# Kernel optimization log

Measured on AMD Instinct MI355X. Metric: run time of the kernel, lower is better.

## Reference

```python
import jax, jax.numpy as jnp
import numpy as np

B, LQ, LK, D, H = 8, 1024, 1024, 1024, 8
DH = D // H  # per-head dim (att_units // num_heads, and V head dim since V = k)
LN_EPS = 1e-5


def setup_inputs() -> dict:
    key = jax.random.key(0)
    ks = jax.random.split(key, 8)
    s = 1.0 / np.sqrt(D)
    return {
        "q": jax.random.normal(ks[0], (B, LQ, D), dtype=jnp.float32),
        "k": jax.random.normal(ks[1], (B, LK, D), dtype=jnp.float32),
        "Wq": jax.random.normal(ks[2], (D, D), dtype=jnp.float32) * s,
        "bq": jnp.zeros((D,), dtype=jnp.float32),
        "Wk": jax.random.normal(ks[3], (D, D), dtype=jnp.float32) * s,
        "bk": jnp.zeros((D,), dtype=jnp.float32),
        "ln_gamma": jnp.ones((D,), dtype=jnp.float32),
        "ln_beta": jnp.zeros((D,), dtype=jnp.float32),
    }


def _layer_norm(x, gamma, beta):
    mu = jnp.mean(x, axis=-1, keepdims=True)
    var = jnp.mean(jnp.square(x - mu), axis=-1, keepdims=True)
    return (x - mu) * jax.lax.rsqrt(var + LN_EPS) * gamma + beta


def reference(q, k, Wq, bq, Wk, bk, ln_gamma, ln_beta):
    # q: [B, LQ, D], k: [B, LK, D]
    Q = q @ Wq + bq                      # [B, LQ, D]
    K = k @ Wk + bk                      # [B, LK, D]
    V = k                                # V is the raw key input (no projection)
    Qh = Q.reshape(B, LQ, H, DH)         # split(att_units//H, -1)+concat(0) == head reshape
    Kh = K.reshape(B, LK, H, DH)
    Vh = V.reshape(B, LK, H, DH)
    sim = jnp.einsum("bqhd,bkhd->bhqk", Qh, Kh) / np.sqrt(DH).astype(np.float32)
    attn = jax.nn.softmax(sim, axis=-1)  # [B, H, LQ, LK]
    att_h = jnp.einsum("bhqk,bkhd->bqhd", attn, Vh).reshape(B, LQ, D)
    att_h = att_h * 0.1 + q * 0.9        # residual blend
    att_h = _layer_norm(att_h, ln_gamma, ln_beta)
    return att_h  # ff_units_list == [] -> ff is None -> ff_h = att_h
```

## Files before the change

kernel.cpp:

```cpp
#include <hip/hip_runtime.h>
#include <hip/hip_bf16.h>
#include <cstdint>

#define BATCH 8
#define SEQ   1024
#define DMODEL 1024
#define NHEAD 8
#define DHEAD 128

using short8 = __attribute__((ext_vector_type(8))) short;
using f32x4  = __attribute__((ext_vector_type(4))) float;
typedef unsigned short u16;

__device__ inline u16 f2bf(float f) {
    union { float f; uint32_t u; } v; v.f = f;
    uint32_t r = (v.u + 0x7FFFu + ((v.u >> 16) & 1u)) >> 16;
    return (u16)r;
}

__device__ inline float exp2_fast(float x) { return __builtin_amdgcn_exp2f(x); }

__device__ inline uint32_t cvtpk_bf16(float a, float b) {
    uint32_t r;
    asm("v_cvt_pk_bf16_f32 %0, %1, %2" : "=v"(r) : "v"(a), "v"(b));
    return r;
}

#define GLL16(g, l)                                                                        \
    __builtin_amdgcn_global_load_lds((__attribute__((address_space(1))) const uint32_t*)(g), \
                                     (__attribute__((address_space(3))) uint32_t*)(l), 16, 0, 0)

__global__ __launch_bounds__(256) void conv_bf16(const float* __restrict__ q,
                                                 u16* __restrict__ dst) {
    size_t e = ((size_t)blockIdx.x * 256 + threadIdx.x) * 8;
    float4 a = *(const float4*)(q + e);
    float4 b = *(const float4*)(q + e + 4);
    uint4 r;
    r.x = cvtpk_bf16(a.x, a.y);
    r.y = cvtpk_bf16(a.z, a.w);
    r.z = cvtpk_bf16(b.x, b.y);
    r.w = cvtpk_bf16(b.z, b.w);
    *(uint4*)(dst + e) = r;
}

__global__ void transpose_conv(const float* __restrict__ Wq,
                               const float* __restrict__ Wk,
                               const float* __restrict__ kin,
                               u16* __restrict__ WqT,
                               u16* __restrict__ WkT,
                               u16* __restrict__ Vt,
                               u16* __restrict__ kb) {
    __shared__ float tile[32][33];
    int z = blockIdx.z;
    const float* src;
    u16* dst;
    u16* sdst = nullptr;
    if (z == 0)      { src = Wq; dst = WqT; }
    else if (z == 1) { src = Wk; dst = WkT; }
    else {
        src  = kin + (size_t)(z - 2) * DMODEL * SEQ;
        dst  = Vt  + (size_t)(z - 2) * DMODEL * SEQ;
        sdst = kb  + (size_t)(z - 2) * DMODEL * SEQ;
    }
    int x  = blockIdx.x * 32 + threadIdx.x;
    int y0 = blockIdx.y * 32;
    for (int i = threadIdx.y; i < 32; i += 8) {
        float v = src[(size_t)(y0 + i) * 1024 + x];
        tile[i][threadIdx.x] = v;
        if (sdst) sdst[(size_t)(y0 + i) * 1024 + x] = f2bf(v);
    }
    __syncthreads();
    int xo  = y0 + threadIdx.x;
    int yo0 = blockIdx.x * 32;
    for (int i = threadIdx.y; i < 32; i += 8)
        dst[(size_t)(yo0 + i) * 1024 + xo] = f2bf(tile[threadIdx.x][i]);
}

__global__ __launch_bounds__(256, 4) void gemm_dual(const u16* __restrict__ Aq,
                                                    const u16* __restrict__ Ak,
                                                    const u16* __restrict__ BTq,
                                                    const u16* __restrict__ BTk,
                                                    const float* __restrict__ biasq,
                                                    const float* __restrict__ biask,
                                                    u16* __restrict__ Outq,
                                                    u16* __restrict__ Outk) {
    __shared__ __align__(16) u16 As[2][128 * 32];
    __shared__ __align__(16) u16 Bs[2][128 * 32];

    int bid = blockIdx.x;
    int half = bid >> 9;
    int b2 = bid & 511;
    const u16* A  = half ? Ak  : Aq;
    const u16* BT = half ? BTk : BTq;
    const float* bias = half ? biask : biasq;
    u16* Out = half ? Outk : Outq;
    float scale = half ? 1.0f : (0.08838834764831845f * 1.4426950408889634f);

    int swz = (b2 & 7) * 64 + (b2 >> 3);
    int mt = swz >> 3, nt = swz & 7;
    int m0 = mt * 128, n0 = nt * 128;

    int t = threadIdx.x, lane = t & 63, w = t >> 6;
    int wm = w >> 1, wn = w & 1;
    int lr = lane & 15, lg = lane >> 4;

    const u16* pa[2];
    const u16* pb[2];
#pragma unroll
    for (int i = 0; i < 2; ++i) {
        int L = (w * 2 + i) * 64 + lane;
        int rp = L >> 3, ss = L & 7;
        int u = ss ^ (rp & 7);
        int row = (rp << 1) | (u >> 2);
        int g = u & 3;
        pa[i] = A  + (size_t)(m0 + row) * 1024 + g * 8;
        pb[i] = BT + (size_t)(n0 + row) * 1024 + g * 8;
    }
    int aoff[4], boff[4];
#pragma unroll
    for (int f = 0; f < 4; ++f) {
        int rowA = wm * 64 + f * 16 + lr;
        int sA = (((rowA & 1) << 2) | lg) ^ ((rowA >> 1) & 7);
        aoff[f] = (rowA >> 1) * 64 + sA * 8;
        int rowB = wn * 64 + f * 16 + lr;
        int sB = (((rowB & 1) << 2) | lg) ^ ((rowB >> 1) & 7);
        boff[f] = (rowB >> 1) * 64 + sB * 8;
    }

    f32x4 acc[4][4] = {};

#define GSTAGE(buf)                                         \
    {                                                       \
        _Pragma("unroll")                                   \
        for (int i = 0; i < 2; ++i) {                       \
            GLL16(pa[i], &As[buf][(w * 2 + i) * 512]);      \
            GLL16(pb[i], &Bs[buf][(w * 2 + i) * 512]);      \
            pa[i] += 32;                                    \
            pb[i] += 32;                                    \
        }                                                   \
    }

    GSTAGE(0);
    __syncthreads();

    int cur = 0;
    for (int k0 = 0; k0 < DMODEL; k0 += 32) {
        if (k0 + 32 < DMODEL) GSTAGE(cur ^ 1);
        short8 af[4], bfr[4];
#pragma unroll
        for (int f = 0; f < 4; ++f) {
            af[f]  = *(const short8*)&As[cur][aoff[f]];
            bfr[f] = *(const short8*)&Bs[cur][boff[f]];
        }
        __builtin_amdgcn_s_setprio(1);
#pragma unroll
        for (int fm = 0; fm < 4; ++fm)
#pragma unroll
            for (int fn = 0; fn < 4; ++fn)
                acc[fm][fn] = __builtin_amdgcn_mfma_f32_16x16x32_bf16(af[fm], bfr[fn], acc[fm][fn], 0, 0, 0);
        __builtin_amdgcn_s_setprio(0);
        __syncthreads();
        cur ^= 1;
    }
#undef GSTAGE

#pragma unroll
    for (int fn = 0; fn < 4; ++fn) {
        int col = n0 + wn * 64 + fn * 16 + lr;
        float bv = bias[col];
#pragma unroll
        for (int fm = 0; fm < 4; ++fm)
#pragma unroll
            for (int j = 0; j < 4; ++j) {
                int row = m0 + wm * 64 + fm * 16 + lg * 4 + j;
                Out[(size_t)row * 1024 + col] = f2bf((acc[fm][fn][j] + bv) * scale);
            }
    }
}

__global__ __launch_bounds__(512, 4) void attn_kernel(const u16* __restrict__ Qb,
                                                      const u16* __restrict__ Kb,
                                                      const u16* __restrict__ Vt,
                                                      float* __restrict__ AO) {
    __shared__ __align__(16) u16 Kbuf[2][64 * 128];
    __shared__ __align__(16) u16 Vbuf[2][128 * 64];
    __shared__ __align__(16) u16 Pl[8][16 * 64];

    int bid = blockIdx.x;
    int swz = (bid & 7) * 64 + (bid >> 3);
    int bh  = swz >> 3;
    int qt  = swz & 7;
    int b = bh >> 3, h = bh & 7;
    int q0 = qt * 128;

    int t = threadIdx.x, lane = t & 63, w = t >> 6;
    int lr = lane & 15, lg = lane >> 4;

    short8 qf[4];
    {
        size_t qbase = (size_t)(b * SEQ + q0 + w * 16 + lr) * 1024 + h * DHEAD;
#pragma unroll
        for (int kk = 0; kk < 4; ++kk)
            qf[kk] = *(const short8*)&Qb[qbase + kk * 32 + lg * 8];
    }

    float m_i = -1e30f, l_loc = 0.f;
    f32x4 o[8] = {};
    u16* Pw = &Pl[w][0];
    const int pwrow = lr * 64;
    const int lx = lr & 7;

#define STAGE(nb, kk0)                                                                   \
    {                                                                                    \
        _Pragma("unroll")                                                                \
        for (int i = 0; i < 2; ++i) {                                                    \
            int g = (w * 2 + i) * 64 + lane;                                             \
            int row = g >> 4, cp = g & 15;                                               \
            int c = cp ^ (row & 7);                                                      \
            const u16* src = Kb + ((size_t)(b * SEQ + (kk0) + row) * 1024 + h * 128 + c * 8); \
            GLL16(src, &Kbuf[nb][(w * 2 + i) * 512]);                                    \
        }                                                                                \
        _Pragma("unroll")                                                                \
        for (int i = 0; i < 2; ++i) {                                                    \
            int g = (w * 2 + i) * 64 + lane;                                             \
            int d = g >> 3, cp = g & 7;                                                  \
            int c = cp ^ (d & 7);                                                        \
            const u16* src = Vt + ((size_t)(bh * 128 + d) * 1024 + (kk0) + c * 8);       \
            GLL16(src, &Vbuf[nb][(w * 2 + i) * 512]);                                    \
        }                                                                                \
    }

    STAGE(0, 0);
    __syncthreads();

    int cur = 0;
    for (int k0 = 0; k0 < SEQ; k0 += 64) {
        if (k0 + 64 < SEQ) STAGE(cur ^ 1, k0 + 64);

        const u16* Kc = &Kbuf[cur][0];
        f32x4 s[4] = {};
        __builtin_amdgcn_s_setprio(1);
#pragma unroll
        for (int fn = 0; fn < 4; ++fn) {
            int krow = (fn * 16 + lr) * 128;
#pragma unroll
            for (int kk = 0; kk < 4; ++kk) {
                short8 kf = *(const short8*)&Kc[krow + (((kk * 4 + lg) ^ lx) << 3)];
                s[fn] = __builtin_amdgcn_mfma_f32_16x16x32_bf16(kf, qf[kk], s[fn], 0, 0, 0);
            }
        }
        __builtin_amdgcn_s_setprio(0);

        float pm0 = fmaxf(fmaxf(s[0][0], s[0][1]), fmaxf(s[0][2], s[0][3]));
        float pm1 = fmaxf(fmaxf(s[1][0], s[1][1]), fmaxf(s[1][2], s[1][3]));
        float pm2 = fmaxf(fmaxf(s[2][0], s[2][1]), fmaxf(s[2][2], s[2][3]));
        float pm3 = fmaxf(fmaxf(s[3][0], s[3][1]), fmaxf(s[3][2], s[3][3]));
        float pmax = fmaxf(fmaxf(pm0, pm1), fmaxf(pm2, pm3));

        if (__any(pmax > m_i + 11.5416f)) {
            float rm = pmax;
            rm = fmaxf(rm, __shfl_xor(rm, 16));
            rm = fmaxf(rm, __shfl_xor(rm, 32));
            float mnew = fmaxf(m_i, rm);
            float alpha = exp2_fast(m_i - mnew);
            m_i = mnew;
            l_loc *= alpha;
#pragma unroll
            for (int db = 0; db < 8; ++db) o[db] *= alpha;
        }

        float p[4][4];
        float ls0 = 0.f, ls1 = 0.f, ls2 = 0.f, ls3 = 0.f;
#pragma unroll
        for (int j = 0; j < 4; ++j) {
            p[0][j] = exp2_fast(s[0][j] - m_i); ls0 += p[0][j];
            p[1][j] = exp2_fast(s[1][j] - m_i); ls1 += p[1][j];
            p[2][j] = exp2_fast(s[2][j] - m_i); ls2 += p[2][j];
            p[3][j] = exp2_fast(s[3][j] - m_i); ls3 += p[3][j];
        }
        l_loc += (ls0 + ls1) + (ls2 + ls3);

#pragma unroll
        for (int fn = 0; fn < 4; ++fn) {
            uint2 pk;
            pk.x = cvtpk_bf16(p[fn][0], p[fn][1]);
            pk.y = cvtpk_bf16(p[fn][2], p[fn][3]);
            int idx = pwrow + (((fn * 2 + (lg >> 1)) ^ lx) << 3) + ((lg & 1) << 2);
            *(uint2*)&Pw[idx] = pk;
        }

        const u16* Vc = &Vbuf[cur][0];
        short8 pf0 = *(const short8*)&Pw[pwrow + ((lg ^ lx) << 3)];
        short8 pf1 = *(const short8*)&Pw[pwrow + (((4 + lg) ^ lx) << 3)];
        __builtin_amdgcn_s_setprio(1);
#pragma unroll
        for (int db = 0; db < 8; ++db) {
            int vr = (db * 16 + lr) * 64;
            short8 v0 = *(const short8*)&Vc[vr + ((lg ^ lx) << 3)];
            short8 v1 = *(const short8*)&Vc[vr + (((4 + lg) ^ lx) << 3)];
            o[db] = __builtin_amdgcn_mfma_f32_16x16x32_bf16(v0, pf0, o[db], 0, 0, 0);
            o[db] = __builtin_amdgcn_mfma_f32_16x16x32_bf16(v1, pf1, o[db], 0, 0, 0);
        }
        __builtin_amdgcn_s_setprio(0);

        __syncthreads();
        cur ^= 1;
    }

    float lt = l_loc;
    lt += __shfl_xor(lt, 16);
    lt += __shfl_xor(lt, 32);
    float inv = 1.f / lt;
    size_t obase = (size_t)(b * SEQ + q0 + w * 16 + lr) * 1024 + h * DHEAD + lg * 4;
#pragma unroll
    for (int db = 0; db < 8; ++db) {
        float4 ov;
        ov.x = o[db][0] * inv;
        ov.y = o[db][1] * inv;
        ov.z = o[db][2] * inv;
        ov.w = o[db][3] * inv;
        *(float4*)&AO[obase + db * 16] = ov;
    }
#undef STAGE
}

__global__ __launch_bounds__(256) void ln_kernel(float* __restrict__ AO,
                                                 const float* __restrict__ qin,
                                                 const float* __restrict__ gamma,
                                                 const float* __restrict__ beta,
                                                 float* __restrict__ out) {
    __shared__ float red[8];
    int row = blockIdx.x;
    int t = threadIdx.x;
    size_t base = (size_t)row * 1024 + t * 4;

    float4 a = *(const float4*)&AO[base];
    float4 qq = *(const float4*)&qin[base];
    float x0 = a.x * 0.1f + qq.x * 0.9f;
    float x1 = a.y * 0.1f + qq.y * 0.9f;
    float x2 = a.z * 0.1f + qq.z * 0.9f;
    float x3 = a.w * 0.1f + qq.w * 0.9f;

    float s  = x0 + x1 + x2 + x3;
    float s2 = x0 * x0 + x1 * x1 + x2 * x2 + x3 * x3;
    for (int d = 1; d < 64; d <<= 1) {
        s  += __shfl_xor(s, d);
        s2 += __shfl_xor(s2, d);
    }
    int w = t >> 6, lane = t & 63;
    if (lane == 0) { red[w] = s; red[4 + w] = s2; }
    __syncthreads();
    s  = red[0] + red[1] + red[2] + red[3];
    s2 = red[4] + red[5] + red[6] + red[7];

    float mu   = s * (1.f / 1024.f);
    float var  = s2 * (1.f / 1024.f) - mu * mu;
    float rstd = rsqrtf(var + 1e-5f);

    float4 g  = *(const float4*)&gamma[t * 4];
    float4 be = *(const float4*)&beta[t * 4];
    float4 o;
    o.x = (x0 - mu) * rstd * g.x + be.x;
    o.y = (x1 - mu) * rstd * g.y + be.y;
    o.z = (x2 - mu) * rstd * g.z + be.z;
    o.w = (x3 - mu) * rstd * g.w + be.w;
    *(float4*)&out[base] = o;
}

extern "C" void kernel_launch(void* const* d_in, const int* in_sizes, int n_in,
                              void* d_out, int out_size, void* d_ws, size_t ws_size,
                              hipStream_t stream) {
    const float* q     = (const float*)d_in[0];
    const float* k     = (const float*)d_in[1];
    const float* Wq    = (const float*)d_in[2];
    const float* bq    = (const float*)d_in[3];
    const float* Wk    = (const float*)d_in[4];
    const float* bk    = (const float*)d_in[5];
    const float* gamma = (const float*)d_in[6];
    const float* beta  = (const float*)d_in[7];
    float* out = (float*)d_out;

    char* ws = (char*)d_ws;
    u16* WqT = (u16*)ws;
    u16* WkT = (u16*)(ws + (size_t)(2  << 20));
    u16* Qb  = (u16*)(ws + (size_t)(4  << 20));
    u16* Kb  = (u16*)(ws + (size_t)(20 << 20));
    u16* Vt  = (u16*)(ws + (size_t)(36 << 20));

    u16* qb = (u16*)d_out;
    u16* kb = qb + (size_t)8 * 1024 * 1024;

    conv_bf16<<<4096, 256, 0, stream>>>(q, qb);

    transpose_conv<<<dim3(32, 32, 2 + BATCH), dim3(32, 8), 0, stream>>>(Wq, Wk, k, WqT, WkT, Vt, kb);

    gemm_dual<<<1024, 256, 0, stream>>>(qb, kb, WqT, WkT, bq, bk, Qb, Kb);

    attn_kernel<<<512, 512, 0, stream>>>(Qb, Kb, Vt, out);

    ln_kernel<<<8192, 256, 0, stream>>>(out, q, gamma, beta, out);
}
```

Baseline: 133.3 us.

## Process two query subtiles per wave to double K/V reuse in attention

Each wave now handles 32 query rows (two 16-row subtiles) instead of 16, so each block covers 256 queries and the grid halves to 256 blocks. Every K and V fragment read from shared memory feeds two MFMAs, which halves LDS traffic and global K/V staging per query. The cost is twice the accumulator registers, so launch bounds drop to 2 blocks per CU, and with only 256 blocks on a 256-CU part there is one block per CU, leaving less latency hiding.

After: 132.7 us. No clear change (-0.5%).

```diff
diff --git a/kernel.cpp b/kernel.cpp
--- a/kernel.cpp
+++ b/kernel.cpp
@@ -178,35 +178,39 @@
     }
 }
 
-__global__ __launch_bounds__(512, 4) void attn_kernel(const u16* __restrict__ Qb,
+__global__ __launch_bounds__(512, 2) void attn_kernel(const u16* __restrict__ Qb,
                                                       const u16* __restrict__ Kb,
                                                       const u16* __restrict__ Vt,
                                                       float* __restrict__ AO) {
     __shared__ __align__(16) u16 Kbuf[2][64 * 128];
     __shared__ __align__(16) u16 Vbuf[2][128 * 64];
-    __shared__ __align__(16) u16 Pl[8][16 * 64];
+    __shared__ __align__(16) u16 Pl[8][2][16 * 64];
 
     int bid = blockIdx.x;
-    int swz = (bid & 7) * 64 + (bid >> 3);
-    int bh  = swz >> 3;
-    int qt  = swz & 7;
+    int swz = (bid & 7) * 32 + (bid >> 3);
+    int bh  = swz >> 2;
+    int qt  = swz & 3;
     int b = bh >> 3, h = bh & 7;
-    int q0 = qt * 128;
+    int q0 = qt * 256;
 
     int t = threadIdx.x, lane = t & 63, w = t >> 6;
     int lr = lane & 15, lg = lane >> 4;
 
-    short8 qf[4];
+    short8 qfA[4], qfB[4];
     {
-        size_t qbase = (size_t)(b * SEQ + q0 + w * 16 + lr) * 1024 + h * DHEAD;
-#pragma unroll
-        for (int kk = 0; kk < 4; ++kk)
-            qf[kk] = *(const short8*)&Qb[qbase + kk * 32 + lg * 8];
-    }
-
-    float m_i = -1e30f, l_loc = 0.f;
-    f32x4 o[8] = {};
-    u16* Pw = &Pl[w][0];
+        size_t qa = (size_t)(b * SEQ + q0 + w * 32 + lr) * 1024 + h * DHEAD;
+        size_t qbB = qa + (size_t)16 * 1024;
+#pragma unroll
+        for (int kk = 0; kk < 4; ++kk) {
+            qfA[kk] = *(const short8*)&Qb[qa  + kk * 32 + lg * 8];
+            qfB[kk] = *(const short8*)&Qb[qbB + kk * 32 + lg * 8];
+        }
+    }
+
+    float mA = -1e30f, lA = 0.f, mB = -1e30f, lB = 0.f;
+    f32x4 oA[8] = {}, oB[8] = {};
+    u16* PwA = &Pl[w][0][0];
+    u16* PwB = &Pl[w][1][0];
     const int pwrow = lr * 64;
     const int lx = lr & 7;
 
@@ -238,7 +242,7 @@
         if (k0 + 64 < SEQ) STAGE(cur ^ 1, k0 + 64);
 
         const u16* Kc = &Kbuf[cur][0];
-        f32x4 s[4] = {};
+        f32x4 sA[4] = {}, sB[4] = {};
         __builtin_amdgcn_s_setprio(1);
 #pragma unroll
         for (int fn = 0; fn < 4; ++fn) {
@@ -246,60 +250,100 @@
 #pragma unroll
             for (int kk = 0; kk < 4; ++kk) {
                 short8 kf = *(const short8*)&Kc[krow + (((kk * 4 + lg) ^ lx) << 3)];
-                s[fn] = __builtin_amdgcn_mfma_f32_16x16x32_bf16(kf, qf[kk], s[fn], 0, 0, 0);
+                sA[fn] = __builtin_amdgcn_mfma_f32_16x16x32_bf16(kf, qfA[kk], sA[fn], 0, 0, 0);
+                sB[fn] = __builtin_amdgcn_mfma_f32_16x16x32_bf16(kf, qfB[kk], sB[fn], 0, 0, 0);
             }
         }
         __builtin_amdgcn_s_setprio(0);
 
-        float pm0 = fmaxf(fmaxf(s[0][0], s[0][1]), fmaxf(s[0][2], s[0][3]));
-        float pm1 = fmaxf(fmaxf(s[1][0], s[1][1]), fmaxf(s[1][2], s[1][3]));
-        float pm2 = fmaxf(fmaxf(s[2][0], s[2][1]), fmaxf(s[2][2], s[2][3]));
-        float pm3 = fmaxf(fmaxf(s[3][0], s[3][1]), fmaxf(s[3][2], s[3][3]));
-        float pmax = fmaxf(fmaxf(pm0, pm1), fmaxf(pm2, pm3));
-
-        if (__any(pmax > m_i + 11.5416f)) {
-            float rm = pmax;
-            rm = fmaxf(rm, __shfl_xor(rm, 16));
-            rm = fmaxf(rm, __shfl_xor(rm, 32));
-            float mnew = fmaxf(m_i, rm);
-            float alpha = exp2_fast(m_i - mnew);
-            m_i = mnew;
-            l_loc *= alpha;
-#pragma unroll
-            for (int db = 0; db < 8; ++db) o[db] *= alpha;
-        }
-
-        float p[4][4];
-        float ls0 = 0.f, ls1 = 0.f, ls2 = 0.f, ls3 = 0.f;
-#pragma unroll
-        for (int j = 0; j < 4; ++j) {
-            p[0][j] = exp2_fast(s[0][j] - m_i); ls0 += p[0][j];
-            p[1][j] = exp2_fast(s[1][j] - m_i); ls1 += p[1][j];
-            p[2][j] = exp2_fast(s[2][j] - m_i); ls2 += p[2][j];
-            p[3][j] = exp2_fast(s[3][j] - m_i); ls3 += p[3][j];
-        }
-        l_loc += (ls0 + ls1) + (ls2 + ls3);
-
-#pragma unroll
-        for (int fn = 0; fn < 4; ++fn) {
-            uint2 pk;
-            pk.x = cvtpk_bf16(p[fn][0], p[fn][1]);
-            pk.y = cvtpk_bf16(p[fn][2], p[fn][3]);
-            int idx = pwrow + (((fn * 2 + (lg >> 1)) ^ lx) << 3) + ((lg & 1) << 2);
-            *(uint2*)&Pw[idx] = pk;
+        {
+            float pm0 = fmaxf(fmaxf(sA[0][0], sA[0][1]), fmaxf(sA[0][2], sA[0][3]));
+            float pm1 = fmaxf(fmaxf(sA[1][0], sA[1][1]), fmaxf(sA[1][2], sA[1][3]));
+            float pm2 = fmaxf(fmaxf(sA[2][0], sA[2][1]), fmaxf(sA[2][2], sA[2][3]));
+            float pm3 = fmaxf(fmaxf(sA[3][0], sA[3][1]), fmaxf(sA[3][2], sA[3][3]));
+            float pmax = fmaxf(fmaxf(pm0, pm1), fmaxf(pm2, pm3));
+            if (__any(pmax > mA + 11.5416f)) {
+                float rm = pmax;
+                rm = fmaxf(rm, __shfl_xor(rm, 16));
+                rm = fmaxf(rm, __shfl_xor(rm, 32));
+                float mnew = fmaxf(mA, rm);
+                float alpha = exp2_fast(mA - mnew);
+                mA = mnew;
+                lA *= alpha;
+#pragma unroll
+                for (int db = 0; db < 8; ++db) oA[db] *= alpha;
+            }
+            float p[4][4];
+            float ls0 = 0.f, ls1 = 0.f, ls2 = 0.f, ls3 = 0.f;
+#pragma unroll
+            for (int j = 0; j < 4; ++j) {
+                p[0][j] = exp2_fast(sA[0][j] - mA); ls0 += p[0][j];
+                p[1][j] = exp2_fast(sA[1][j] - mA); ls1 += p[1][j];
+                p[2][j] = exp2_fast(sA[2][j] - mA); ls2 += p[2][j];
+                p[3][j] = exp2_fast(sA[3][j] - mA); ls3 += p[3][j];
+            }
+            lA += (ls0 + ls1) + (ls2 + ls3);
+#pragma unroll
+            for (int fn = 0; fn < 4; ++fn) {
+                uint2 pk;
+                pk.x = cvtpk_bf16(p[fn][0], p[fn][1]);
+                pk.y = cvtpk_bf16(p[fn][2], p[fn][3]);
+                int idx = pwrow + (((fn * 2 + (lg >> 1)) ^ lx) << 3) + ((lg & 1) << 2);
+                *(uint2*)&PwA[idx] = pk;
+            }
+        }
+        {
+            float pm0 = fmaxf(fmaxf(sB[0][0], sB[0][1]), fmaxf(sB[0][2], sB[0][3]));
+            float pm1 = fmaxf(fmaxf(sB[1][0], sB[1][1]), fmaxf(sB[1][2], sB[1][3]));
+            float pm2 = fmaxf(fmaxf(sB[2][0], sB[2][1]), fmaxf(sB[2][2], sB[2][3]));
+            float pm3 = fmaxf(fmaxf(sB[3][0], sB[3][1]), fmaxf(sB[3][2], sB[3][3]));
+            float pmax = fmaxf(fmaxf(pm0, pm1), fmaxf(pm2, pm3));
+            if (__any(pmax > mB + 11.5416f)) {
+                float rm = pmax;
+                rm = fmaxf(rm, __shfl_xor(rm, 16));
+                rm = fmaxf(rm, __shfl_xor(rm, 32));
+                float mnew = fmaxf(mB, rm);
+                float alpha = exp2_fast(mB - mnew);
+                mB = mnew;
+                lB *= alpha;
+#pragma unroll
+                for (int db = 0; db < 8; ++db) oB[db] *= alpha;
+            }
+            float p[4][4];
+            float ls0 = 0.f, ls1 = 0.f, ls2 = 0.f, ls3 = 0.f;
+#pragma unroll
+            for (int j = 0; j < 4; ++j) {
+                p[0][j] = exp2_fast(sB[0][j] - mB); ls0 += p[0][j];
+                p[1][j] = exp2_fast(sB[1][j] - mB); ls1 += p[1][j];
+                p[2][j] = exp2_fast(sB[2][j] - mB); ls2 += p[2][j];
+                p[3][j] = exp2_fast(sB[3][j] - mB); ls3 += p[3][j];
+            }
+            lB += (ls0 + ls1) + (ls2 + ls3);
+#pragma unroll
+            for (int fn = 0; fn < 4; ++fn) {
+                uint2 pk;
+                pk.x = cvtpk_bf16(p[fn][0], p[fn][1]);
+                pk.y = cvtpk_bf16(p[fn][2], p[fn][3]);
+                int idx = pwrow + (((fn * 2 + (lg >> 1)) ^ lx) << 3) + ((lg & 1) << 2);
+                *(uint2*)&PwB[idx] = pk;
+            }
         }
 
         const u16* Vc = &Vbuf[cur][0];
-        short8 pf0 = *(const short8*)&Pw[pwrow + ((lg ^ lx) << 3)];
-        short8 pf1 = *(const short8*)&Pw[pwrow + (((4 + lg) ^ lx) << 3)];
+        short8 pfA0 = *(const short8*)&PwA[pwrow + ((lg ^ lx) << 3)];
+        short8 pfA1 = *(const short8*)&PwA[pwrow + (((4 + lg) ^ lx) << 3)];
+        short8 pfB0 = *(const short8*)&PwB[pwrow + ((lg ^ lx) << 3)];
+        short8 pfB1 = *(const short8*)&PwB[pwrow + (((4 + lg) ^ lx) << 3)];
         __builtin_amdgcn_s_setprio(1);
 #pragma unroll
         for (int db = 0; db < 8; ++db) {
             int vr = (db * 16 + lr) * 64;
             short8 v0 = *(const short8*)&Vc[vr + ((lg ^ lx) << 3)];
             short8 v1 = *(const short8*)&Vc[vr + (((4 + lg) ^ lx) << 3)];
-            o[db] = __builtin_amdgcn_mfma_f32_16x16x32_bf16(v0, pf0, o[db], 0, 0, 0);
-            o[db] = __builtin_amdgcn_mfma_f32_16x16x32_bf16(v1, pf1, o[db], 0, 0, 0);
+            oA[db] = __builtin_amdgcn_mfma_f32_16x16x32_bf16(v0, pfA0, oA[db], 0, 0, 0);
+            oA[db] = __builtin_amdgcn_mfma_f32_16x16x32_bf16(v1, pfA1, oA[db], 0, 0, 0);
+            oB[db] = __builtin_amdgcn_mfma_f32_16x16x32_bf16(v0, pfB0, oB[db], 0, 0, 0);
+            oB[db] = __builtin_amdgcn_mfma_f32_16x16x32_bf16(v1, pfB1, oB[db], 0, 0, 0);
         }
         __builtin_amdgcn_s_setprio(0);
 
@@ -307,19 +351,30 @@
         cur ^= 1;
     }
 
-    float lt = l_loc;
-    lt += __shfl_xor(lt, 16);
-    lt += __shfl_xor(lt, 32);
-    float inv = 1.f / lt;
-    size_t obase = (size_t)(b * SEQ + q0 + w * 16 + lr) * 1024 + h * DHEAD + lg * 4;
+    float ltA = lA;
+    ltA += __shfl_xor(ltA, 16);
+    ltA += __shfl_xor(ltA, 32);
+    float invA = 1.f / ltA;
+    float ltB = lB;
+    ltB += __shfl_xor(ltB, 16);
+    ltB += __shfl_xor(ltB, 32);
+    float invB = 1.f / ltB;
+    size_t obaseA = (size_t)(b * SEQ + q0 + w * 32 + lr) * 1024 + h * DHEAD + lg * 4;
+    size_t obaseB = obaseA + (size_t)16 * 1024;
 #pragma unroll
     for (int db = 0; db < 8; ++db) {
         float4 ov;
-        ov.x = o[db][0] * inv;
-        ov.y = o[db][1] * inv;
-        ov.z = o[db][2] * inv;
-        ov.w = o[db][3] * inv;
-        *(float4*)&AO[obase + db * 16] = ov;
+        ov.x = oA[db][0] * invA;
+        ov.y = oA[db][1] * invA;
+        ov.z = oA[db][2] * invA;
+        ov.w = oA[db][3] * invA;
+        *(float4*)&AO[obaseA + db * 16] = ov;
+        float4 ow;
+        ow.x = oB[db][0] * invB;
+        ow.y = oB[db][1] * invB;
+        ow.z = oB[db][2] * invB;
+        ow.w = oB[db][3] * invB;
+        *(float4*)&AO[obaseB + db * 16] = ow;
     }
 #undef STAGE
 }
@@ -396,7 +451,7 @@
 
     gemm_dual<<<1024, 256, 0, stream>>>(qb, kb, WqT, WkT, bq, bk, Qb, Kb);
 
-    attn_kernel<<<512, 512, 0, stream>>>(Qb, Kb, Vt, out);
+    attn_kernel<<<256, 512, 0, stream>>>(Qb, Kb, Vt, out);
 
     ln_kernel<<<8192, 256, 0, stream>>>(out, q, gamma, beta, out);
 }
```
